# Kernel tuning notes

Hardware: AMD Instinct MI355X
Metric: run time of the kernel (lower is better)

## Reference

```python
import jax, jax.numpy as jnp
import numpy as np

N, IN_DIM, H, D = 4096, 512, 8, 64
NEG = -1e9  # additive mask value for non-edges


def setup_inputs() -> dict:
    key = jax.random.key(0)
    k1, k2, k3, k4, k5, k6 = jax.random.split(key, 6)
    data = jax.random.normal(k1, (N, IN_DIM), dtype=jnp.float32)
    r = jax.random.uniform(k2, (N, N), dtype=jnp.float32)
    connectivity = jnp.where(r < 0.05, 0.0, NEG).astype(jnp.float32)
    # xavier-uniform-ish init for params
    lim_w = float(np.sqrt(6.0 / (IN_DIM + H * D)))
    W = jax.random.uniform(k3, (H * D, IN_DIM), jnp.float32, -lim_w, lim_w)
    b = jnp.zeros((H * D,), jnp.float32)
    lim_p = float(np.sqrt(6.0 / (H * D + 1)))
    src_proj = jax.random.uniform(k4, (1, H, D), jnp.float32, -lim_p, lim_p)
    trg_proj = jax.random.uniform(k5, (1, H, D), jnp.float32, -lim_p, lim_p)
    return {"data": data, "connectivity": connectivity, "W": W, "b": b,
            "src_proj": src_proj, "trg_proj": trg_proj}


def reference(data, connectivity, W, b, src_proj, trg_proj):
    # dropout is identity in eval mode (reference is deterministic)
    data1 = (data @ W.T + b).reshape(N, H, D)          # (N,H,D)
    src = jnp.einsum('nhd,xhd->nh', data1, src_proj)   # (N,H)
    trg = jnp.einsum('nhd,xhd->nh', data1, trg_proj)   # (N,H)
    # scores: (H,N,1) + (H,1,N) broadcast outer-sum
    e = src.T[:, :, None] + trg.T[:, None, :]          # (H,N,N)
    e = jnp.where(e >= 0, e, 0.01 * e)                 # LeakyReLU(0.01)
    e = e + connectivity[None, :, :]                   # additive mask
    scores = jax.nn.softmax(e, axis=-1)                # (H,N,N)
    # bmm over heads: (H,N,N) x (H,N,D) -> (H,N,D)
    out = jnp.einsum('hnm,hmd->hnd', scores, data1.transpose(1, 0, 2))
    out = out.transpose(1, 0, 2).reshape(N, H * D)     # concat=True
    return out
```

## Files before the change

### kernel.cpp

```cpp
#include <hip/hip_runtime.h>
#include <hip/hip_bf16.h>

#define NN 4096
#define IN_DIM 512
#define NH 8
#define DD 64
#define HD 512
#define LOG2E 1.4426950408889634f
#define CAST_WGS 2304
#define SCAN_WGS 1024


typedef __attribute__((ext_vector_type(8))) short short8;
typedef __attribute__((ext_vector_type(4))) float f32x4;

typedef __attribute__((address_space(1))) const unsigned int gu32;
typedef __attribute__((address_space(3))) unsigned int lu32;

static __device__ __forceinline__ unsigned short f2bf(float x) {
    __hip_bfloat16 h = __float2bfloat16(x);
    return *reinterpret_cast<unsigned short*>(&h);
}

static __device__ __forceinline__ unsigned cvtpk_bf16(float a, float b) {
    unsigned r;
    asm("v_cvt_pk_bf16_f32 %0, %1, %2" : "=v"(r) : "v"(a), "v"(b));
    return r;
}

static __device__ __forceinline__ void gload_lds16(const void* g, void* l) {
    __builtin_amdgcn_global_load_lds((gu32*)g, (lu32*)l, 16, 0, 0);
}

__global__ __launch_bounds__(256) void k_cast_scan(const float* __restrict__ inA,
                                                   unsigned short* __restrict__ outA,
                                                   int n4A,
                                                   const float* __restrict__ inB,
                                                   unsigned short* __restrict__ outB,
                                                   int n4B,
                                                   const float* __restrict__ conn,
                                                   unsigned long long* __restrict__ bm) {
    if (blockIdx.x >= CAST_WGS) {
        const int lane = threadIdx.x & 63;
        const int w = threadIdx.x >> 6;
        const int row = (blockIdx.x - CAST_WGS) * 4 + w;
        const float* crow = conn + (size_t)row * NN;
        unsigned long long keep = 0;
#pragma unroll 8
        for (int t = 0; t < 64; t++) {
            float c = crow[t * 64 + lane];
            unsigned long long m = __ballot(c == 0.0f);
            if (lane == t) keep = m;
        }
        bm[(size_t)row * 64 + lane] = keep;
        return;
    }
    int t = blockIdx.x * 256 + threadIdx.x;
    const float* in;
    unsigned short* out;
    if (t < n4A) {
        in = inA; out = outA;
    } else {
        t -= n4A;
        if (t >= n4B) return;
        in = inB; out = outB;
    }
    float4 v = ((const float4*)in)[t];
    ushort4 o;
    o.x = f2bf(v.x); o.y = f2bf(v.y); o.z = f2bf(v.z); o.w = f2bf(v.w);
    ((ushort4*)out)[t] = o;
}

__global__ __launch_bounds__(512) void k_gemm_fused(const unsigned short* __restrict__ Ab,
                                                    const unsigned short* __restrict__ Wb,
                                                    const float* __restrict__ bias,
                                                    const float* __restrict__ sp,
                                                    const float* __restrict__ tp,
                                                    unsigned short* __restrict__ d1t,
                                                    float* __restrict__ srcT,
                                                    float* __restrict__ trgT) {
    __shared__ f32x4 cbuf[4][4 * 64];
    const int lane = threadIdx.x & 63;
    const int w8 = threadIdx.x >> 6;
    const int w  = w8 & 3;
    const int kh = w8 >> 2;
    const int col = lane & 15;
    const int quad = lane >> 4;
    const int koff = quad * 8 + kh * 256;
    const int h = blockIdx.x;
    const int m0 = h * 64;
    const int n0 = blockIdx.y * 64;

    const short8* ap  = (const short8*)(Ab + (size_t)(n0 + w * 16 + col) * IN_DIM + koff);
    const short8* bp0 = (const short8*)(Wb + (size_t)(m0 +  0 + col) * IN_DIM + koff);
    const short8* bp1 = (const short8*)(Wb + (size_t)(m0 + 16 + col) * IN_DIM + koff);
    const short8* bp2 = (const short8*)(Wb + (size_t)(m0 + 32 + col) * IN_DIM + koff);
    const short8* bp3 = (const short8*)(Wb + (size_t)(m0 + 48 + col) * IN_DIM + koff);

    f32x4 acc0 = {0.f, 0.f, 0.f, 0.f}, acc1 = acc0, acc2 = acc0, acc3 = acc0;

#pragma unroll 8
    for (int ks = 0; ks < 8; ks++) {
        short8 a  = ap[ks * 4];
        short8 b0 = bp0[ks * 4];
        short8 b1 = bp1[ks * 4];
        short8 b2 = bp2[ks * 4];
        short8 b3 = bp3[ks * 4];
        acc0 = __builtin_amdgcn_mfma_f32_16x16x32_bf16(a, b0, acc0, 0, 0, 0);
        acc1 = __builtin_amdgcn_mfma_f32_16x16x32_bf16(a, b1, acc1, 0, 0, 0);
        acc2 = __builtin_amdgcn_mfma_f32_16x16x32_bf16(a, b2, acc2, 0, 0, 0);
        acc3 = __builtin_amdgcn_mfma_f32_16x16x32_bf16(a, b3, acc3, 0, 0, 0);
    }

    if (kh == 1) {
        cbuf[w][0 * 64 + lane] = acc0;
        cbuf[w][1 * 64 + lane] = acc1;
        cbuf[w][2 * 64 + lane] = acc2;
        cbuf[w][3 * 64 + lane] = acc3;
    }
    __syncthreads();
    if (kh == 1) return;
    acc0 += cbuf[w][0 * 64 + lane];
    acc1 += cbuf[w][1 * 64 + lane];
    acc2 += cbuf[w][2 * 64 + lane];
    acc3 += cbuf[w][3 * 64 + lane];

    const int rbase = n0 + w * 16 + quad * 4;
    const int jt  = (n0 >> 5) + (w >> 1);
    const int kqf = ((w & 1) << 1) + (quad >> 1);
    const int half = quad & 1;
    f32x4 accs[4] = {acc0, acc1, acc2, acc3};
    float ps[4] = {0.f, 0.f, 0.f, 0.f};
    float pt[4] = {0.f, 0.f, 0.f, 0.f};
#pragma unroll
    for (int mt = 0; mt < 4; mt++) {
        const int m = m0 + mt * 16 + col;
        const float bv  = bias[m];
        const float spv = sp[m];
        const float tpv = tp[m];
        ushort4 pack;
        unsigned short* pk = (unsigned short*)&pack;
#pragma unroll
        for (int r = 0; r < 4; r++) {
            float v = accs[mt][r] + bv;
            pk[r] = f2bf(v);
            ps[r] += v * spv;
            pt[r] += v * tpv;
        }
        size_t boff = ((((size_t)(h * 128 + jt) * 4 + mt) * 64 + kqf * 16 + col) << 4)
                    + ((size_t)half << 3);
        *(ushort4*)((char*)d1t + boff) = pack;
    }
#pragma unroll
    for (int off = 1; off <= 8; off <<= 1) {
#pragma unroll
        for (int r = 0; r < 4; r++) {
            ps[r] += __shfl_xor(ps[r], off, 64);
            pt[r] += __shfl_xor(pt[r], off, 64);
        }
    }
    if (col < 4)
        srcT[(size_t)h * NN + rbase + col] = ps[col] * LOG2E;
    else if (col < 8)
        trgT[(size_t)h * NN + rbase + col - 4] = pt[col - 4] * LOG2E;
}

#define FLASH_STEP(STEPN, RBASE, WDST, BQU, TAU, TBU, BQL, TAL, TBL)               \
    do {                                                                           \
        const int s1_ = ((STEPN) + 1 < 32) ? (STEPN) + 1 : 31;                     \
        const uint4* gsrc_ = gw + (size_t)s1_ * 1024;                              \
        gload_lds16(gsrc_, (WDST));                                                \
        gload_lds16(gsrc_ + 512, (WDST) + 8192);                                   \
        BQL = *(const uint4*)(bp + s1_ * 4);                                       \
        _Pragma("unroll")                                                          \
        for (int j_ = 0; j_ < 4; j_++) {                                           \
            TAL[j_] = *(const float4*)(tpp + (s1_ * 4 + j_) * 32);                 \
            TBL[j_] = *(const float4*)(tpp + (s1_ * 4 + j_) * 32 + 4);             \
        }                                                                          \
        const unsigned bqa_[4] = {BQU.x, BQU.y, BQU.z, BQU.w};                     \
        _Pragma("unroll")                                                          \
        for (int jtl_ = 0; jtl_ < 4; jtl_++) {                                     \
            const unsigned bits_ = (bqa_[jtl_] >> (kq * 8)) & 0xffu;               \
            const float tv_[8] = {TAU[jtl_].x, TAU[jtl_].y, TAU[jtl_].z,           \
                                  TAU[jtl_].w, TBU[jtl_].x, TBU[jtl_].y,           \
                                  TBU[jtl_].z, TBU[jtl_].w};                       \
            float p_[8];                                                           \
            _Pragma("unroll")                                                      \
            for (int r_ = 0; r_ < 8; r_++) {                                       \
                float e_ = s + tv_[r_];                                            \
                e_ = fmaxf(e_, 0.01f * e_);                                        \
                float pv_ = __builtin_amdgcn_exp2f(e_);                            \
                pv_ *= (float)((bits_ >> r_) & 1u);                                \
                p_[r_] = pv_;                                                      \
            }                                                                      \
            union { uint4 u; short8 s8; } pk_;                                     \
            pk_.u.x = cvtpk_bf16(p_[0], p_[1]);                                    \
            pk_.u.y = cvtpk_bf16(p_[2], p_[3]);                                    \
            pk_.u.z = cvtpk_bf16(p_[4], p_[5]);                                    \
            pk_.u.w = cvtpk_bf16(p_[6], p_[7]);                                    \
            const char* cb_ = (RBASE) + jtl_ * 4096 + lane * 16;                   \
            short8 v0_ = *(const short8*)(cb_);                                    \
            short8 v1_ = *(const short8*)(cb_ + 1024);                             \
            short8 v2_ = *(const short8*)(cb_ + 2048);                             \
            short8 v3_ = *(const short8*)(cb_ + 3072);                             \
            __builtin_amdgcn_s_setprio(1);                                         \
            acc0 = __builtin_amdgcn_mfma_f32_16x16x32_bf16(pk_.s8, v0_, acc0, 0, 0, 0); \
            acc1 = __builtin_amdgcn_mfma_f32_16x16x32_bf16(pk_.s8, v1_, acc1, 0, 0, 0); \
            acc2 = __builtin_amdgcn_mfma_f32_16x16x32_bf16(pk_.s8, v2_, acc2, 0, 0, 0); \
            acc3 = __builtin_amdgcn_mfma_f32_16x16x32_bf16(pk_.s8, v3_, acc3, 0, 0, 0); \
            asum = __builtin_amdgcn_mfma_f32_16x16x32_bf16(pk_.s8, ONES, asum, 0, 0, 0); \
            __builtin_amdgcn_s_setprio(0);                                         \
        }                                                                          \
        __syncthreads();                                                           \
    } while (0)

__global__ __launch_bounds__(512) void k_flash(const unsigned* __restrict__ bm32,
                                               const float* __restrict__ srcT,
                                               const float* __restrict__ trgT,
                                               const unsigned short* __restrict__ d1t,
                                               float* __restrict__ out) {
    __shared__ char vt[2][16384];

    const int t = threadIdx.x;
    const int lane = t & 63;
    const int w = t >> 6;
    const int col = lane & 15;
    const int kq = lane >> 4;
    const int i0 = blockIdx.x * 128;
    const int h = blockIdx.y;
    const int m = i0 + w * 16 + col;

    const float s = srcT[(size_t)h * NN + m];
    const unsigned* bp = bm32 + (size_t)m * 128;
    const float* tpp = trgT + (size_t)h * NN + kq * 8;
    const uint4* gv = (const uint4*)d1t + (size_t)h * 32768;
    const uint4* gw = gv + w * 64 + lane;
    char* l0 = vt[0] + w * 1024;
    char* l1 = vt[1] + w * 1024;
    const short8 ONES = {0x3F80, 0x3F80, 0x3F80, 0x3F80, 0x3F80, 0x3F80, 0x3F80, 0x3F80};

    f32x4 acc0 = {0.f, 0.f, 0.f, 0.f}, acc1 = acc0, acc2 = acc0, acc3 = acc0;
    f32x4 asum = acc0;

    uint4 bqA, bqB;
    float4 tAA[4], tBA[4], tAB[4], tBB[4];

    gload_lds16(gw, l0);
    gload_lds16(gw + 512, l0 + 8192);
    bqA = *(const uint4*)(bp);
#pragma unroll
    for (int j = 0; j < 4; j++) {
        tAA[j] = *(const float4*)(tpp + j * 32);
        tBA[j] = *(const float4*)(tpp + j * 32 + 4);
    }
    __syncthreads();

    for (int it = 0; it < 16; it++) {
        FLASH_STEP(2 * it,     vt[0], l1, bqA, tAA, tBA, bqB, tAB, tBB);
        FLASH_STEP(2 * it + 1, vt[1], l0, bqB, tAB, tBB, bqA, tAA, tBA);
    }

    f32x4 accs[4] = {acc0, acc1, acc2, acc3};
#pragma unroll
    for (int r = 0; r < 4; r++) {
        const int row = i0 + w * 16 + kq * 4 + r;
        const float dv = asum[r];
        const float inv = (dv > 0.f) ? (1.f / dv) : 0.f;
        float* op = out + (size_t)row * HD + h * 64;
#pragma unroll
        for (int dt = 0; dt < 4; dt++)
            op[dt * 16 + col] = accs[dt][r] * inv;
    }
}

extern "C" void kernel_launch(void* const* d_in, const int* in_sizes, int n_in,
                              void* d_out, int out_size, void* d_ws, size_t ws_size,
                              hipStream_t stream) {
    const float* data = (const float*)d_in[0];
    const float* conn = (const float*)d_in[1];
    const float* W    = (const float*)d_in[2];
    const float* bias = (const float*)d_in[3];
    const float* sp   = (const float*)d_in[4];
    const float* tp   = (const float*)d_in[5];
    float* out = (float*)d_out;

    unsigned short* d1t = (unsigned short*)d_ws;
    unsigned short* Ab  = d1t + (size_t)HD * NN;
    unsigned short* Wb  = Ab + (size_t)NN * IN_DIM;
    float* srcT = (float*)(Wb + (size_t)HD * IN_DIM);
    float* trgT = srcT + NH * NN;
    unsigned long long* bm = (unsigned long long*)(trgT + NH * NN);

    const int n4A = NN * IN_DIM / 4;
    const int n4B = HD * IN_DIM / 4;
    k_cast_scan<<<dim3(CAST_WGS + SCAN_WGS), 256, 0, stream>>>(data, Ab, n4A, W, Wb, n4B,
                                                               conn, bm);
    k_gemm_fused<<<dim3(NH, NN / 64), 512, 0, stream>>>(Ab, Wb, bias, sp, tp,
                                                        d1t, srcT, trgT);
    k_flash<<<dim3(NN / 128, NH), 512, 0, stream>>>((const unsigned*)bm, srcT, trgT, d1t, out);
}
```

Measured before the change: 184.9 us.

## Shrink flash blocks to 64 rows and replace syncthreads with partial vmcnt waits

The attention kernel now launches 512 workgroups of 256 threads, each covering 64 rows of one head with head-interleaved block indexing. Every wave issues four LDS-direct loads per step to fill the shared V tile. The full __syncthreads is replaced by a partial s_waitcnt vmcnt plus s_barrier with sched_barriers, so the next tile's global loads can stay in flight during the MFMA loop. The risks are a fragile hand-picked vmcnt count and twice as many reloads of the shared V tiles across blocks.

```diff
diff --git a/kernel.cpp b/kernel.cpp
--- a/kernel.cpp
+++ b/kernel.cpp
@@ -165,18 +165,23 @@
         trgT[(size_t)h * NN + rbase + col - 4] = pt[col - 4] * LOG2E;
 }
 
-#define FLASH_STEP(STEPN, RBASE, WDST, BQU, TAU, TBU, BQL, TAL, TBL)               \
+#define FLASH_STEP(STEPN, RBUF, WBUF, BQU, TAU, TBU, BQL, TAL, TBL)                \
     do {                                                                           \
         const int s1_ = ((STEPN) + 1 < 32) ? (STEPN) + 1 : 31;                     \
-        const uint4* gsrc_ = gw + (size_t)s1_ * 1024;                              \
-        gload_lds16(gsrc_, (WDST));                                                \
-        gload_lds16(gsrc_ + 512, (WDST) + 8192);                                   \
+        const uint4* gs_ = gw + (size_t)s1_ * 1024;                                \
+        char* wd_ = (WBUF) + w * 1024;                                             \
+        gload_lds16(gs_,       wd_);                                               \
+        gload_lds16(gs_ + 256, wd_ + 4096);                                        \
+        gload_lds16(gs_ + 512, wd_ + 8192);                                        \
+        gload_lds16(gs_ + 768, wd_ + 12288);                                       \
+        __builtin_amdgcn_sched_barrier(0);                                         \
         BQL = *(const uint4*)(bp + s1_ * 4);                                       \
         _Pragma("unroll")                                                          \
         for (int j_ = 0; j_ < 4; j_++) {                                           \
             TAL[j_] = *(const float4*)(tpp + (s1_ * 4 + j_) * 32);                 \
             TBL[j_] = *(const float4*)(tpp + (s1_ * 4 + j_) * 32 + 4);             \
         }                                                                          \
+        __builtin_amdgcn_sched_barrier(0);                                         \
         const unsigned bqa_[4] = {BQU.x, BQU.y, BQU.z, BQU.w};                     \
         _Pragma("unroll")                                                          \
         for (int jtl_ = 0; jtl_ < 4; jtl_++) {                                     \
@@ -198,7 +203,7 @@
             pk_.u.y = cvtpk_bf16(p_[2], p_[3]);                                    \
             pk_.u.z = cvtpk_bf16(p_[4], p_[5]);                                    \
             pk_.u.w = cvtpk_bf16(p_[6], p_[7]);                                    \
-            const char* cb_ = (RBASE) + jtl_ * 4096 + lane * 16;                   \
+            const char* cb_ = (RBUF) + jtl_ * 4096 + lane * 16;                    \
             short8 v0_ = *(const short8*)(cb_);                                    \
             short8 v1_ = *(const short8*)(cb_ + 1024);                             \
             short8 v2_ = *(const short8*)(cb_ + 2048);                             \
@@ -211,10 +216,13 @@
             asum = __builtin_amdgcn_mfma_f32_16x16x32_bf16(pk_.s8, ONES, asum, 0, 0, 0); \
             __builtin_amdgcn_s_setprio(0);                                         \
         }                                                                          \
-        __syncthreads();                                                           \
+        asm volatile("s_waitcnt vmcnt(9)" ::: "memory");                           \
+        __builtin_amdgcn_sched_barrier(0);                                         \
+        __builtin_amdgcn_s_barrier();                                              \
+        __builtin_amdgcn_sched_barrier(0);                                         \
     } while (0)
 
-__global__ __launch_bounds__(512) void k_flash(const unsigned* __restrict__ bm32,
+__global__ __launch_bounds__(256) void k_flash(const unsigned* __restrict__ bm32,
                                                const float* __restrict__ srcT,
                                                const float* __restrict__ trgT,
                                                const unsigned short* __restrict__ d1t,
@@ -226,8 +234,9 @@
     const int w = t >> 6;
     const int col = lane & 15;
     const int kq = lane >> 4;
-    const int i0 = blockIdx.x * 128;
-    const int h = blockIdx.y;
+    const int bid = blockIdx.x;
+    const int h = bid & 7;
+    const int i0 = (bid >> 3) * 64;
     const int m = i0 + w * 16 + col;
 
     const float s = srcT[(size_t)h * NN + m];
@@ -235,8 +244,6 @@
     const float* tpp = trgT + (size_t)h * NN + kq * 8;
     const uint4* gv = (const uint4*)d1t + (size_t)h * 32768;
     const uint4* gw = gv + w * 64 + lane;
-    char* l0 = vt[0] + w * 1024;
-    char* l1 = vt[1] + w * 1024;
     const short8 ONES = {0x3F80, 0x3F80, 0x3F80, 0x3F80, 0x3F80, 0x3F80, 0x3F80, 0x3F80};
 
     f32x4 acc0 = {0.f, 0.f, 0.f, 0.f}, acc1 = acc0, acc2 = acc0, acc3 = acc0;
@@ -245,20 +252,31 @@
     uint4 bqA, bqB;
     float4 tAA[4], tBA[4], tAB[4], tBB[4];
 
-    gload_lds16(gw, l0);
-    gload_lds16(gw + 512, l0 + 8192);
+    {
+        char* wd0 = vt[0] + w * 1024;
+        gload_lds16(gw,       wd0);
+        gload_lds16(gw + 256, wd0 + 4096);
+        gload_lds16(gw + 512, wd0 + 8192);
+        gload_lds16(gw + 768, wd0 + 12288);
+    }
+    __builtin_amdgcn_sched_barrier(0);
     bqA = *(const uint4*)(bp);
 #pragma unroll
     for (int j = 0; j < 4; j++) {
         tAA[j] = *(const float4*)(tpp + j * 32);
         tBA[j] = *(const float4*)(tpp + j * 32 + 4);
     }
-    __syncthreads();
+    __builtin_amdgcn_sched_barrier(0);
+    asm volatile("s_waitcnt vmcnt(9)" ::: "memory");
+    __builtin_amdgcn_sched_barrier(0);
+    __builtin_amdgcn_s_barrier();
+    __builtin_amdgcn_sched_barrier(0);
 
     for (int it = 0; it < 16; it++) {
-        FLASH_STEP(2 * it,     vt[0], l1, bqA, tAA, tBA, bqB, tAB, tBB);
-        FLASH_STEP(2 * it + 1, vt[1], l0, bqB, tAB, tBB, bqA, tAA, tBA);
-    }
+        FLASH_STEP(2 * it,     vt[0], vt[1], bqA, tAA, tBA, bqB, tAB, tBB);
+        FLASH_STEP(2 * it + 1, vt[1], vt[0], bqB, tAB, tBB, bqA, tAA, tBA);
+    }
+    asm volatile("s_waitcnt vmcnt(0)" ::: "memory");
 
     f32x4 accs[4] = {acc0, acc1, acc2, acc3};
 #pragma unroll
@@ -297,5 +315,5 @@
                                                                conn, bm);
     k_gemm_fused<<<dim3(NH, NN / 64), 512, 0, stream>>>(Ab, Wb, bias, sp, tp,
                                                         d1t, srcT, trgT);
-    k_flash<<<dim3(NN / 128, NH), 512, 0, stream>>>((const unsigned*)bm, srcT, trgT, d1t, out);
-}
+    k_flash<<<dim3(512), 256, 0, stream>>>((const unsigned*)bm, srcT, trgT, d1t, out);
+}
```

Result: no change. 188.0 us (+1.7%).
